# Performance work log

Measured on AMD Instinct MI355X. Metric: run time of the kernel, lower is better.

## Reference

```python
import jax, jax.numpy as jnp
import numpy as np

LOG_EPS = -50.0  # clip_weights lower bound assumption (avoid -inf log-weights)

B, T, P, D, DOBS = 32, 64, 2048, 32, 16


def setup_inputs() -> dict:
    key = jax.random.key(0)
    k_obs, k_p0, k_A, k_ls, k_C = jax.random.split(key, 5)
    observations = jax.random.normal(k_obs, (B, T, DOBS), dtype=jnp.float32)
    init_particles = jax.random.normal(k_p0, (B, P, D), dtype=jnp.float32)
    # stable-ish linear-Gaussian transition params
    A = 0.9 * jnp.eye(D, dtype=jnp.float32) + 0.02 * jax.random.normal(k_A, (D, D), dtype=jnp.float32)
    b = jnp.zeros((D,), dtype=jnp.float32)
    log_sigma = -1.0 + 0.1 * jax.random.normal(k_ls, (D,), dtype=jnp.float32)
    C = 0.3 * jax.random.normal(k_C, (DOBS, D), dtype=jnp.float32)
    log_r = jnp.zeros((DOBS,), dtype=jnp.float32)
    return {"observations": observations, "init_particles": init_particles,
            "A": A, "b": b, "log_sigma": log_sigma, "C": C, "log_r": log_r}


def _pf_scan(observations, init_particles, A, b, log_sigma, C, log_r):
    Bv, Tv, dim_obs = observations.shape
    Pv = init_particles.shape[1]
    base_key = jax.random.key(42)
    # initial weights: ones/P, as in get_initial_state (normalized to log-uniform in step)
    w0 = jnp.full((Bv, Pv, 1), 1.0 / Pv, dtype=init_particles.dtype)
    obs_t = jnp.swapaxes(observations, 0, 1)  # [T,B,obs]
    log2pi = jnp.log(2.0 * jnp.pi).astype(init_particles.dtype)

    def step(carry, xs):
        particles, weights = carry
        t, y = xs
        k = jax.random.fold_in(base_key, t)
        k_res, k_noise = jax.random.split(k)
        # _normalize: log-space normalize + clip
        w = weights - jax.scipy.special.logsumexp(weights, axis=1, keepdims=True)
        w = jnp.maximum(w, LOG_EPS)
        # _resample: categorical over particles, batched gather
        idx = jax.random.categorical(k_res, w[..., 0], shape=(Pv, Bv)).T  # [B,P] int
        particles = jnp.take_along_axis(particles, idx[..., None], axis=1)
        # _forward: linear-Gaussian transition x' = A x + b + sigma*eps
        noise = jax.random.normal(k_noise, particles.shape, dtype=particles.dtype)
        particles = jnp.einsum('bpd,ed->bpe', particles, A) + b + noise * jnp.exp(log_sigma)
        # _measurement: log N(y; C x, diag(exp(log_r)^2))  -> [B,P,1]
        mean = jnp.einsum('bpd,od->bpo', particles, C)
        resid = (y[:, None, :] - mean) * jnp.exp(-log_r)
        logw = (-0.5 * jnp.sum(resid * resid, axis=-1)
                - jnp.sum(log_r) - 0.5 * dim_obs * log2pi)
        weights = logw[..., None]
        return (particles, weights), (particles, weights)

    (_, _), (pseq, wseq) = jax.lax.scan(step, (init_particles, w0),
                                        (jnp.arange(Tv), obs_t))
    # [T,B,...] -> [B,T,...]
    return jnp.swapaxes(pseq, 0, 1), jnp.swapaxes(wseq, 0, 1)


def reference(observations, init_particles, A, b, log_sigma, C, log_r):
    return _pf_scan(observations, init_particles, A, b, log_sigma, C, log_r)
```

## Files before the change

kernel.cpp:

```cpp
#include <hip/hip_runtime.h>
#include <math.h>

#define Bb 32
#define Tt 64
#define Pp 2048
#define Dd 32
#define NOBS 16

__device__ __forceinline__ unsigned rotl32(unsigned v, int r) {
  return (v << r) | (v >> (32 - r));
}

__device__ __forceinline__ void tf2x32(unsigned k0, unsigned k1,
                                       unsigned c0, unsigned c1,
                                       unsigned& r0, unsigned& r1) {
  unsigned k2 = k0 ^ k1 ^ 0x1BD11BDAu;
  unsigned x0 = c0 + k0;
  unsigned x1 = c1 + k1;
#define TF_ROUND(R) { x0 += x1; x1 = rotl32(x1, (R)); x1 ^= x0; }
  TF_ROUND(13) TF_ROUND(15) TF_ROUND(26) TF_ROUND(6)
  x0 += k1; x1 += k2 + 1u;
  TF_ROUND(17) TF_ROUND(29) TF_ROUND(16) TF_ROUND(24)
  x0 += k2; x1 += k0 + 2u;
  TF_ROUND(13) TF_ROUND(15) TF_ROUND(26) TF_ROUND(6)
  x0 += k0; x1 += k1 + 3u;
  TF_ROUND(17) TF_ROUND(29) TF_ROUND(16) TF_ROUND(24)
  x0 += k1; x1 += k2 + 4u;
  TF_ROUND(13) TF_ROUND(15) TF_ROUND(26) TF_ROUND(6)
  x0 += k2; x1 += k0 + 5u;
#undef TF_ROUND
  r0 = x0; r1 = x1;
}

__device__ __forceinline__ float logf_cr(float x) { return (float)log((double)x); }
__device__ __forceinline__ float expf_cr(float x) { return (float)exp((double)x); }

__device__ __forceinline__ float gumbel_exact(unsigned bits) {
  float fl = __uint_as_float(0x3f800000u | (bits >> 9)) - 1.0f;
  float u  = __fadd_rn(fl, 1.17549435e-38f);
  float il = logf_cr(u);
  return -logf_cr(-il);
}

__device__ __forceinline__ float gumbel_fast(unsigned bits) {
  float fl = __uint_as_float(0x3f800000u | (bits >> 9)) - 1.0f;
  if (fl > 0.999877929f) return gumbel_exact(bits);
  float u  = fl + 1.17549435e-38f;
  float t  = -__log2f(u);
  return fmaf(-0.69314718056f, __log2f(t), 0.3665129205816643f);
}

__device__ __forceinline__ float erfinv_xla(float x) {
  float nxx = __fmul_rn(-x, x);
  float l1p;
  if (fabsf(nxx) < 1e-4f) {
    l1p = __fmul_rn(__fadd_rn(__fmul_rn(-0.5f, nxx), 1.0f), nxx);
  } else {
    l1p = logf_cr(__fadd_rn(1.0f, nxx));
  }
  float w = -l1p;
  float p;
  if (w < 5.0f) {
    float ww = __fsub_rn(w, 2.5f);
    p = 2.81022636e-08f;
    p = __fadd_rn(3.43273939e-07f,  __fmul_rn(p, ww));
    p = __fadd_rn(-3.5233877e-06f,  __fmul_rn(p, ww));
    p = __fadd_rn(-4.39150654e-06f, __fmul_rn(p, ww));
    p = __fadd_rn(0.00021858087f,   __fmul_rn(p, ww));
    p = __fadd_rn(-0.00125372503f,  __fmul_rn(p, ww));
    p = __fadd_rn(-0.00417768164f,  __fmul_rn(p, ww));
    p = __fadd_rn(0.246640727f,     __fmul_rn(p, ww));
    p = __fadd_rn(1.50140941f,      __fmul_rn(p, ww));
  } else {
    float ww = __fsub_rn(sqrtf(w), 3.0f);
    p = -0.000200214257f;
    p = __fadd_rn(0.000100950558f,  __fmul_rn(p, ww));
    p = __fadd_rn(0.00134934322f,   __fmul_rn(p, ww));
    p = __fadd_rn(-0.00367342844f,  __fmul_rn(p, ww));
    p = __fadd_rn(0.00573950773f,   __fmul_rn(p, ww));
    p = __fadd_rn(-0.0076224613f,   __fmul_rn(p, ww));
    p = __fadd_rn(0.00943887047f,   __fmul_rn(p, ww));
    p = __fadd_rn(1.00167406f,      __fmul_rn(p, ww));
    p = __fadd_rn(2.83297682f,      __fmul_rn(p, ww));
  }
  return __fmul_rn(p, x);
}

__global__ __launch_bounds__(256) void norm_kernel(float* __restrict__ wseq,
                                                   int t) {
  __shared__ float lw[Pp];
  __shared__ float red[256];
  __shared__ float rr[128];
  __shared__ float sh_mx, sh_lse;
  int b = blockIdx.x;
  int tid = threadIdx.x;
  const float* src = wseq + ((size_t)b * Tt + (t - 1)) * Pp;
  float loc[8];
  for (int k = 0; k < 8; ++k) {
    int j = tid + k * 256;
    float v = (t == 0) ? 0.00048828125f : src[j];
    lw[j] = v; loc[k] = v;
  }
  float m = loc[0];
  for (int k = 1; k < 8; ++k) m = fmaxf(m, loc[k]);
  red[tid] = m;
  __syncthreads();
  if (tid == 0) {
    float mm = red[0];
    for (int k = 1; k < 256; ++k) mm = fmaxf(mm, red[k]);
    sh_mx = mm;
  }
  __syncthreads();
  float mx = sh_mx;
  if (tid < 128) {
    int base = (tid >> 3) * 128 + (tid & 7);
    float r = expf_cr(__fsub_rn(lw[base], mx));
    for (int i = 1; i < 16; ++i)
      r = __fadd_rn(r, expf_cr(__fsub_rn(lw[base + 8 * i], mx)));
    rr[tid] = r;
  }
  __syncthreads();
  if (tid < 64) {
    float s = __fadd_rn(rr[2 * tid], rr[2 * tid + 1]);
    for (int off = 1; off <= 32; off <<= 1)
      s = __fadd_rn(s, __shfl_xor(s, off));
    if (tid == 0) sh_lse = __fadd_rn(logf_cr(s), mx);
  }
  __syncthreads();
  float lse = sh_lse;
  float* dst = wseq + ((size_t)b * Tt + t) * Pp;
  for (int k = 0; k < 8; ++k) {
    int j = tid + k * 256;
    dst[j] = fmaxf(__fsub_rn(lw[j], lse), -50.0f);
  }
}

__global__ __launch_bounds__(256) void cat_kernel(const float* __restrict__ wseq,
                                                  float* __restrict__ pseq,
                                                  int t) {
  __shared__ float wlds[Pp];
  int b = blockIdx.y;
  int tid = threadIdx.x;
  const float* wn = wseq + ((size_t)b * Tt + t) * Pp;
  for (int k = 0; k < Pp / 256; ++k)
    wlds[tid + k * 256] = wn[tid + k * 256];
  __syncthreads();

  unsigned kt0, kt1, kr0, kr1;
  tf2x32(0u, 42u, 0u, (unsigned)t, kt0, kt1);
  tf2x32(kt0, kt1, 0u, 0u, kr0, kr1);

  int wave = tid >> 6, lane = tid & 63;
  int i = blockIdx.x * 4 + wave;
  unsigned base_m = ((unsigned)i * Bb + (unsigned)b) * (unsigned)Pp;

  float vf[32];
  float best = -INFINITY;
#pragma unroll
  for (int jj = 0; jj < 32; ++jj) {
    unsigned b0, b1;
    tf2x32(kr0, kr1, 0u, base_m + (unsigned)(jj * 64 + lane), b0, b1);
    float v = __fadd_rn(gumbel_fast(b0 ^ b1), wlds[jj * 64 + lane]);
    vf[jj] = v;
    best = fmaxf(best, v);
  }
  for (int off = 1; off <= 32; off <<= 1)
    best = fmaxf(best, __shfl_xor(best, off));
  float cut = best - 0.125f;

  unsigned mask = 0u;
#pragma unroll
  for (int jj = 0; jj < 32; ++jj)
    mask |= (vf[jj] >= cut) ? (1u << jj) : 0u;

  float bv = -INFINITY;
  int bj = 0x7fffffff;
  while (mask) {
    int jj = __builtin_ctz(mask);
    mask &= mask - 1u;
    int j = jj * 64 + lane;
    unsigned b0, b1;
    tf2x32(kr0, kr1, 0u, base_m + (unsigned)j, b0, b1);
    float v = __fadd_rn(gumbel_exact(b0 ^ b1), wlds[j]);
    if (v > bv) { bv = v; bj = j; }
  }
  for (int off = 1; off <= 32; off <<= 1) {
    float ov = __shfl_xor(bv, off);
    int   oj = __shfl_xor(bj, off);
    if (ov > bv || (ov == bv && oj < bj)) { bv = ov; bj = oj; }
  }
  if (lane == 0)
    ((int*)pseq)[(((size_t)b * Tt + t) * Pp + i) * Dd] = bj;
}

__global__ __launch_bounds__(256) void fwd_kernel(
    const float* __restrict__ prev,
    float* __restrict__ pseq,
    float* __restrict__ wseq,
    const float* __restrict__ obs,
    const float* __restrict__ Amat,
    const float* __restrict__ bvec,
    const float* __restrict__ log_sigma,
    const float* __restrict__ Cmat,
    const float* __restrict__ log_r,
    int t) {
  int gid = blockIdx.x * 256 + threadIdx.x;
  int b = gid >> 11;
  int p = gid & (Pp - 1);

  unsigned kt0, kt1, kn0, kn1;
  tf2x32(0u, 42u, 0u, (unsigned)t, kt0, kt1);
  tf2x32(kt0, kt1, 0u, 1u, kn0, kn1);

  size_t slot = (((size_t)b * Tt + t) * Pp + p) * Dd;
  int src_p = ((const int*)pseq)[slot];
  const float* xsrc = (t == 0)
      ? (prev + ((size_t)b * Pp + src_p) * Dd)
      : (prev + (((size_t)b * Tt + (t - 1)) * Pp + src_p) * Dd);
  float x[Dd];
  for (int d = 0; d < Dd; ++d) x[d] = xsrc[d];

  float xn[Dd];
  unsigned base_m = ((unsigned)b * Pp + (unsigned)p) * (unsigned)Dd;
  for (int e = 0; e < Dd; ++e) {
    float acc = 0.f;
    for (int d = 0; d < Dd; ++d) acc = fmaf(x[d], Amat[e * Dd + d], acc);
    unsigned b0, b1;
    tf2x32(kn0, kn1, 0u, base_m + (unsigned)e, b0, b1);
    unsigned bits = b0 ^ b1;
    float fl = __uint_as_float(0x3f800000u | (bits >> 9)) - 1.0f;
    float u  = __fadd_rn(__fmul_rn(fl, 2.0f), -0x1.fffffep-1f);
    float n  = __fmul_rn(1.41421356f, erfinv_xla(u));
    xn[e] = __fadd_rn(__fadd_rn(acc, bvec[e]),
                      __fmul_rn(n, expf_cr(log_sigma[e])));
  }

  float* pdst = pseq + slot;
  for (int e = 0; e < Dd; ++e) pdst[e] = xn[e];

  const float* y = obs + ((size_t)b * Tt + t) * NOBS;
  float aa[NOBS];
  for (int o = 0; o < NOBS; ++o) {
    float macc = 0.f;
    for (int d = 0; d < Dd; ++d) macc = fmaf(xn[d], Cmat[o * Dd + d], macc);
    float r = __fmul_rn(__fsub_rn(y[o], macc), expf_cr(-log_r[o]));
    aa[o] = __fmul_rn(r, r);
  }
  float r8[8], l8[8];
  for (int o = 0; o < 8; ++o) {
    r8[o] = __fadd_rn(aa[o], aa[o + 8]);
    l8[o] = __fadd_rn(log_r[o], log_r[o + 8]);
  }
  float S = __fadd_rn(
      __fadd_rn(__fadd_rn(r8[0], r8[1]), __fadd_rn(r8[2], r8[3])),
      __fadd_rn(__fadd_rn(r8[4], r8[5]), __fadd_rn(r8[6], r8[7])));
  float slr = __fadd_rn(
      __fadd_rn(__fadd_rn(l8[0], l8[1]), __fadd_rn(l8[2], l8[3])),
      __fadd_rn(__fadd_rn(l8[4], l8[5]), __fadd_rn(l8[6], l8[7])));
  const float c_term = 8.0f * (float)1.8378770664093453;
  float logw = __fsub_rn(__fsub_rn(__fmul_rn(-0.5f, S), slr), c_term);
  wseq[((size_t)b * Tt + t) * Pp + p] = logw;
}

extern "C" void kernel_launch(void* const* d_in, const int* in_sizes, int n_in,
                              void* d_out, int out_size, void* d_ws, size_t ws_size,
                              hipStream_t stream) {
  (void)in_sizes; (void)n_in; (void)out_size; (void)d_ws; (void)ws_size;
  const float* obs       = (const float*)d_in[0];
  const float* init_p    = (const float*)d_in[1];
  const float* Amat      = (const float*)d_in[2];
  const float* bvec      = (const float*)d_in[3];
  const float* log_sigma = (const float*)d_in[4];
  const float* Cmat      = (const float*)d_in[5];
  const float* log_r     = (const float*)d_in[6];

  float* pseq = (float*)d_out;
  float* wseq = pseq + (size_t)Bb * Tt * Pp * Dd;

  for (int t = 0; t < Tt; ++t) {
    norm_kernel<<<Bb, 256, 0, stream>>>(wseq, t);
    cat_kernel<<<dim3(Pp / 4, Bb), 256, 0, stream>>>(wseq, pseq, t);
    fwd_kernel<<<(Bb * Pp) / 256, 256, 0, stream>>>(
        t == 0 ? init_p : pseq, pseq, wseq,
        obs, Amat, bvec, log_sigma, Cmat, log_r, t);
  }
}
```

Before: 23.28 ms.

## Prune resampling candidates whose log-weight cannot win the Gumbel-max draw

The normalization kernel now keeps only particles whose normalized log-weight is within a fixed margin (20.45) of the maximum. It compacts them with a shared-memory atomic counter into a (weight, index) workspace list, along with a per-batch count. The categorical kernel loads only those active entries and runs the Threefry and Gumbel evaluations over whole 64-wide chunks of them, padding the tail with -inf. The aim is to skip most of the per-candidate RNG and Gumbel cost when the weights are peaked. Results stay exact only if the margin exceeds the spread of Gumbel noise that float uniforms can produce; atomic ordering is nondeterministic, so ties are broken explicitly by index.

Result: no change. 23.62 ms (+1.4%).

```diff
diff --git a/kernel.cpp b/kernel.cpp
--- a/kernel.cpp
+++ b/kernel.cpp
@@ -86,12 +86,15 @@
   return __fmul_rn(p, x);
 }
 
-__global__ __launch_bounds__(256) void norm_kernel(float* __restrict__ wseq,
+__global__ __launch_bounds__(256) void norm_kernel(const float* __restrict__ wseq,
+                                                   float2* __restrict__ act,
+                                                   int* __restrict__ counts,
                                                    int t) {
   __shared__ float lw[Pp];
   __shared__ float red[256];
   __shared__ float rr[128];
   __shared__ float sh_mx, sh_lse;
+  __shared__ int s_cnt;
   int b = blockIdx.x;
   int tid = threadIdx.x;
   const float* src = wseq + ((size_t)b * Tt + (t - 1)) * Pp;
@@ -126,24 +129,37 @@
       s = __fadd_rn(s, __shfl_xor(s, off));
     if (tid == 0) sh_lse = __fadd_rn(logf_cr(s), mx);
   }
+  if (tid == 0) s_cnt = 0;
   __syncthreads();
   float lse = sh_lse;
-  float* dst = wseq + ((size_t)b * Tt + t) * Pp;
+  float thr = __fsub_rn(__fsub_rn(mx, lse), 20.45f);
+  float2* abase = act + (size_t)b * Pp;
   for (int k = 0; k < 8; ++k) {
     int j = tid + k * 256;
-    dst[j] = fmaxf(__fsub_rn(lw[j], lse), -50.0f);
-  }
-}
-
-__global__ __launch_bounds__(256) void cat_kernel(const float* __restrict__ wseq,
+    float wn = fmaxf(__fsub_rn(lw[j], lse), -50.0f);
+    if (wn >= thr) {
+      int pos = atomicAdd(&s_cnt, 1);
+      abase[pos] = make_float2(wn, __int_as_float(j));
+    }
+  }
+  __syncthreads();
+  if (tid == 0) counts[b] = s_cnt;
+}
+
+__global__ __launch_bounds__(256) void cat_kernel(const float2* __restrict__ act,
+                                                  const int* __restrict__ counts,
                                                   float* __restrict__ pseq,
                                                   int t) {
-  __shared__ float wlds[Pp];
+  __shared__ float2 alds[Pp];
   int b = blockIdx.y;
   int tid = threadIdx.x;
-  const float* wn = wseq + ((size_t)b * Tt + t) * Pp;
-  for (int k = 0; k < Pp / 256; ++k)
-    wlds[tid + k * 256] = wn[tid + k * 256];
+  int n_act = counts[b];
+  int nchunk = (n_act + 63) >> 6;
+  int tot = nchunk << 6;
+  const float2* abase = act + (size_t)b * Pp;
+  for (int k = tid; k < tot; k += 256)
+    alds[k] = (k < n_act) ? abase[k]
+                          : make_float2(-INFINITY, __int_as_float(0x7fffffff));
   __syncthreads();
 
   unsigned kt0, kt1, kr0, kr1;
@@ -157,12 +173,17 @@
   float vf[32];
   float best = -INFINITY;
 #pragma unroll
-  for (int jj = 0; jj < 32; ++jj) {
-    unsigned b0, b1;
-    tf2x32(kr0, kr1, 0u, base_m + (unsigned)(jj * 64 + lane), b0, b1);
-    float v = __fadd_rn(gumbel_fast(b0 ^ b1), wlds[jj * 64 + lane]);
-    vf[jj] = v;
-    best = fmaxf(best, v);
+  for (int c = 0; c < 32; ++c) {
+    if (c < nchunk) {
+      float2 aw = alds[c * 64 + lane];
+      unsigned b0, b1;
+      tf2x32(kr0, kr1, 0u, base_m + (unsigned)__float_as_int(aw.y), b0, b1);
+      float v = __fadd_rn(gumbel_fast(b0 ^ b1), aw.x);
+      vf[c] = v;
+      best = fmaxf(best, v);
+    } else {
+      vf[c] = -INFINITY;
+    }
   }
   for (int off = 1; off <= 32; off <<= 1)
     best = fmaxf(best, __shfl_xor(best, off));
@@ -170,19 +191,20 @@
 
   unsigned mask = 0u;
 #pragma unroll
-  for (int jj = 0; jj < 32; ++jj)
-    mask |= (vf[jj] >= cut) ? (1u << jj) : 0u;
+  for (int c = 0; c < 32; ++c)
+    mask |= (vf[c] >= cut) ? (1u << c) : 0u;
 
   float bv = -INFINITY;
   int bj = 0x7fffffff;
   while (mask) {
-    int jj = __builtin_ctz(mask);
+    int c = __builtin_ctz(mask);
     mask &= mask - 1u;
-    int j = jj * 64 + lane;
+    float2 aw = alds[c * 64 + lane];
+    int j = __float_as_int(aw.y);
     unsigned b0, b1;
     tf2x32(kr0, kr1, 0u, base_m + (unsigned)j, b0, b1);
-    float v = __fadd_rn(gumbel_exact(b0 ^ b1), wlds[j]);
-    if (v > bv) { bv = v; bj = j; }
+    float v = __fadd_rn(gumbel_exact(b0 ^ b1), aw.x);
+    if (v > bv || (v == bv && j < bj)) { bv = v; bj = j; }
   }
   for (int off = 1; off <= 32; off <<= 1) {
     float ov = __shfl_xor(bv, off);
@@ -265,7 +287,7 @@
 extern "C" void kernel_launch(void* const* d_in, const int* in_sizes, int n_in,
                               void* d_out, int out_size, void* d_ws, size_t ws_size,
                               hipStream_t stream) {
-  (void)in_sizes; (void)n_in; (void)out_size; (void)d_ws; (void)ws_size;
+  (void)in_sizes; (void)n_in; (void)out_size; (void)ws_size;
   const float* obs       = (const float*)d_in[0];
   const float* init_p    = (const float*)d_in[1];
   const float* Amat      = (const float*)d_in[2];
@@ -277,9 +299,12 @@
   float* pseq = (float*)d_out;
   float* wseq = pseq + (size_t)Bb * Tt * Pp * Dd;
 
+  int*    counts = (int*)d_ws;
+  float2* act    = (float2*)((char*)d_ws + 256);
+
   for (int t = 0; t < Tt; ++t) {
-    norm_kernel<<<Bb, 256, 0, stream>>>(wseq, t);
-    cat_kernel<<<dim3(Pp / 4, Bb), 256, 0, stream>>>(wseq, pseq, t);
+    norm_kernel<<<Bb, 256, 0, stream>>>(wseq, act, counts, t);
+    cat_kernel<<<dim3(Pp / 4, Bb), 256, 0, stream>>>(act, counts, pseq, t);
     fwd_kernel<<<(Bb * Pp) / 256, 256, 0, stream>>>(
         t == 0 ? init_p : pseq, pseq, wseq,
         obs, Amat, bvec, log_sigma, Cmat, log_r, t);
```

## Prefilter Gumbel-max candidates via precomputed integer thresholds on random bits

Applied to the files above, without the earlier changes.

The normalize kernel now writes the normalized log-weights plus, for each particle, the smallest raw random-bit value whose Gumbel sample would push weight+Gumbel above a fixed cutoff. The categorical kernel then only generates Threefry bits and does an integer compare per candidate, computing exact Gumbel logs only for the few that pass, instead of a fast Gumbel for every candidate. If no candidate reaches the cutoff, a full exact rescan runs as a fallback, so results stay exact. PRNG key derivation per timestep also moves to the host and is passed as kernel arguments, at the cost of an extra workspace array and more double-precision math in the normalize kernel.

New measurement: 23.23 ms. Within noise of the previous version (-0.2%).

```diff
diff --git a/kernel.cpp b/kernel.cpp
--- a/kernel.cpp
+++ b/kernel.cpp
@@ -6,6 +6,8 @@
 #define Pp 2048
 #define Dd 32
 #define NOBS 16
+
+#define CUTF (-2.3f)
 
 __device__ __forceinline__ unsigned rotl32(unsigned v, int r) {
   return (v << r) | (v >> (32 - r));
@@ -32,6 +34,27 @@
   r0 = x0; r1 = x1;
 }
 
+static inline void tf2x32_host(unsigned k0, unsigned k1,
+                               unsigned c0, unsigned c1,
+                               unsigned& r0, unsigned& r1) {
+  unsigned k2 = k0 ^ k1 ^ 0x1BD11BDAu;
+  unsigned x0 = c0 + k0;
+  unsigned x1 = c1 + k1;
+#define TF_ROUND(R) { x0 += x1; x1 = (x1 << (R)) | (x1 >> (32 - (R))); x1 ^= x0; }
+  TF_ROUND(13) TF_ROUND(15) TF_ROUND(26) TF_ROUND(6)
+  x0 += k1; x1 += k2 + 1u;
+  TF_ROUND(17) TF_ROUND(29) TF_ROUND(16) TF_ROUND(24)
+  x0 += k2; x1 += k0 + 2u;
+  TF_ROUND(13) TF_ROUND(15) TF_ROUND(26) TF_ROUND(6)
+  x0 += k0; x1 += k1 + 3u;
+  TF_ROUND(17) TF_ROUND(29) TF_ROUND(16) TF_ROUND(24)
+  x0 += k1; x1 += k2 + 4u;
+  TF_ROUND(13) TF_ROUND(15) TF_ROUND(26) TF_ROUND(6)
+  x0 += k2; x1 += k0 + 5u;
+#undef TF_ROUND
+  r0 = x0; r1 = x1;
+}
+
 __device__ __forceinline__ float logf_cr(float x) { return (float)log((double)x); }
 __device__ __forceinline__ float expf_cr(float x) { return (float)exp((double)x); }
 
@@ -40,14 +63,6 @@
   float u  = __fadd_rn(fl, 1.17549435e-38f);
   float il = logf_cr(u);
   return -logf_cr(-il);
-}
-
-__device__ __forceinline__ float gumbel_fast(unsigned bits) {
-  float fl = __uint_as_float(0x3f800000u | (bits >> 9)) - 1.0f;
-  if (fl > 0.999877929f) return gumbel_exact(bits);
-  float u  = fl + 1.17549435e-38f;
-  float t  = -__log2f(u);
-  return fmaf(-0.69314718056f, __log2f(t), 0.3665129205816643f);
 }
 
 __device__ __forceinline__ float erfinv_xla(float x) {
@@ -86,7 +101,9 @@
   return __fmul_rn(p, x);
 }
 
-__global__ __launch_bounds__(256) void norm_kernel(float* __restrict__ wseq,
+__global__ __launch_bounds__(256) void norm_kernel(const float* __restrict__ wseq,
+                                                   float* __restrict__ wn_out,
+                                                   unsigned* __restrict__ vs_out,
                                                    int t) {
   __shared__ float lw[Pp];
   __shared__ float red[256];
@@ -128,67 +145,88 @@
   }
   __syncthreads();
   float lse = sh_lse;
-  float* dst = wseq + ((size_t)b * Tt + t) * Pp;
+  float* wdst = wn_out + (size_t)b * Pp;
+  unsigned* vdst = vs_out + (size_t)b * Pp;
   for (int k = 0; k < 8; ++k) {
     int j = tid + k * 256;
-    dst[j] = fmaxf(__fsub_rn(lw[j], lse), -50.0f);
-  }
-}
-
-__global__ __launch_bounds__(256) void cat_kernel(const float* __restrict__ wseq,
+    float wn = fmaxf(__fsub_rn(lw[j], lse), -50.0f);
+    wdst[j] = wn;
+    double g_req = (double)CUTF - (double)wn;
+    double U  = exp(-exp(-g_req));
+    double Um = U - 1e-4;
+    unsigned V;
+    if (!(Um > 0.0)) {
+      V = 0u;
+    } else {
+      double mth = ceil(Um * 8388608.0);
+      V = (mth >= 8388608.0) ? 0xFFFFFFFFu : (((unsigned)mth) << 9);
+    }
+    vdst[j] = V;
+  }
+}
+
+__global__ __launch_bounds__(256) void cat_kernel(const float* __restrict__ wn_ws,
+                                                  const unsigned* __restrict__ vs_ws,
                                                   float* __restrict__ pseq,
-                                                  int t) {
+                                                  int t, unsigned kr0, unsigned kr1) {
   __shared__ float wlds[Pp];
+  __shared__ unsigned vlds[Pp];
   int b = blockIdx.y;
   int tid = threadIdx.x;
-  const float* wn = wseq + ((size_t)b * Tt + t) * Pp;
-  for (int k = 0; k < Pp / 256; ++k)
-    wlds[tid + k * 256] = wn[tid + k * 256];
-  __syncthreads();
-
-  unsigned kt0, kt1, kr0, kr1;
-  tf2x32(0u, 42u, 0u, (unsigned)t, kt0, kt1);
-  tf2x32(kt0, kt1, 0u, 0u, kr0, kr1);
+  const float*    wsrc = wn_ws + (size_t)b * Pp;
+  const unsigned* vsrc = vs_ws + (size_t)b * Pp;
+  for (int k = 0; k < Pp / 256; ++k) {
+    wlds[tid + k * 256] = wsrc[tid + k * 256];
+    vlds[tid + k * 256] = vsrc[tid + k * 256];
+  }
+  __syncthreads();
 
   int wave = tid >> 6, lane = tid & 63;
   int i = blockIdx.x * 4 + wave;
   unsigned base_m = ((unsigned)i * Bb + (unsigned)b) * (unsigned)Pp;
 
-  float vf[32];
-  float best = -INFINITY;
-#pragma unroll
-  for (int jj = 0; jj < 32; ++jj) {
+  unsigned mask = 0u;
+#pragma unroll 4
+  for (int c = 0; c < 32; ++c) {
     unsigned b0, b1;
-    tf2x32(kr0, kr1, 0u, base_m + (unsigned)(jj * 64 + lane), b0, b1);
-    float v = __fadd_rn(gumbel_fast(b0 ^ b1), wlds[jj * 64 + lane]);
-    vf[jj] = v;
-    best = fmaxf(best, v);
-  }
-  for (int off = 1; off <= 32; off <<= 1)
-    best = fmaxf(best, __shfl_xor(best, off));
-  float cut = best - 0.125f;
-
-  unsigned mask = 0u;
-#pragma unroll
-  for (int jj = 0; jj < 32; ++jj)
-    mask |= (vf[jj] >= cut) ? (1u << jj) : 0u;
+    tf2x32(kr0, kr1, 0u, base_m + (unsigned)(c * 64 + lane), b0, b1);
+    unsigned bits = b0 ^ b1;
+    if (bits >= vlds[c * 64 + lane]) mask |= (1u << c);
+  }
 
   float bv = -INFINITY;
   int bj = 0x7fffffff;
   while (mask) {
-    int jj = __builtin_ctz(mask);
+    int c = __builtin_ctz(mask);
     mask &= mask - 1u;
-    int j = jj * 64 + lane;
+    int j = c * 64 + lane;
     unsigned b0, b1;
     tf2x32(kr0, kr1, 0u, base_m + (unsigned)j, b0, b1);
     float v = __fadd_rn(gumbel_exact(b0 ^ b1), wlds[j]);
-    if (v > bv) { bv = v; bj = j; }
+    if (v > bv || (v == bv && j < bj)) { bv = v; bj = j; }
   }
   for (int off = 1; off <= 32; off <<= 1) {
     float ov = __shfl_xor(bv, off);
     int   oj = __shfl_xor(bj, off);
     if (ov > bv || (ov == bv && oj < bj)) { bv = ov; bj = oj; }
   }
+
+  if (!(bv >= CUTF)) {
+    bv = -INFINITY; bj = 0x7fffffff;
+    for (int c = 0; c < 32; ++c) {
+      int j = c * 64 + lane;
+      unsigned b0, b1;
+      tf2x32(kr0, kr1, 0u, base_m + (unsigned)j, b0, b1);
+      float v = __fadd_rn(gumbel_exact(b0 ^ b1), wlds[j]);
+      if (v > bv || (v == bv && j < bj)) { bv = v; bj = j; }
+    }
+    for (int off = 1; off <= 32; off <<= 1) {
+      float ov = __shfl_xor(bv, off);
+      int   oj = __shfl_xor(bj, off);
+      if (ov > bv || (ov == bv && oj < bj)) { bv = ov; bj = oj; }
+    }
+  }
+
   if (lane == 0)
     ((int*)pseq)[(((size_t)b * Tt + t) * Pp + i) * Dd] = bj;
 }
@@ -203,14 +241,10 @@
     const float* __restrict__ log_sigma,
     const float* __restrict__ Cmat,
     const float* __restrict__ log_r,
-    int t) {
+    int t, unsigned kn0, unsigned kn1) {
   int gid = blockIdx.x * 256 + threadIdx.x;
   int b = gid >> 11;
   int p = gid & (Pp - 1);
-
-  unsigned kt0, kt1, kn0, kn1;
-  tf2x32(0u, 42u, 0u, (unsigned)t, kt0, kt1);
-  tf2x32(kt0, kt1, 0u, 1u, kn0, kn1);
 
   size_t slot = (((size_t)b * Tt + t) * Pp + p) * Dd;
   int src_p = ((const int*)pseq)[slot];
@@ -265,7 +299,7 @@
 extern "C" void kernel_launch(void* const* d_in, const int* in_sizes, int n_in,
                               void* d_out, int out_size, void* d_ws, size_t ws_size,
                               hipStream_t stream) {
-  (void)in_sizes; (void)n_in; (void)out_size; (void)d_ws; (void)ws_size;
+  (void)in_sizes; (void)n_in; (void)out_size; (void)ws_size;
   const float* obs       = (const float*)d_in[0];
   const float* init_p    = (const float*)d_in[1];
   const float* Amat      = (const float*)d_in[2];
@@ -277,11 +311,19 @@
   float* pseq = (float*)d_out;
   float* wseq = pseq + (size_t)Bb * Tt * Pp * Dd;
 
+  float*    wn = (float*)d_ws;
+  unsigned* vs = (unsigned*)((char*)d_ws + (size_t)Bb * Pp * 4);
+
   for (int t = 0; t < Tt; ++t) {
-    norm_kernel<<<Bb, 256, 0, stream>>>(wseq, t);
-    cat_kernel<<<dim3(Pp / 4, Bb), 256, 0, stream>>>(wseq, pseq, t);
+    unsigned kt0, kt1, kr0, kr1, kn0, kn1;
+    tf2x32_host(0u, 42u, 0u, (unsigned)t, kt0, kt1);
+    tf2x32_host(kt0, kt1, 0u, 0u, kr0, kr1);
+    tf2x32_host(kt0, kt1, 0u, 1u, kn0, kn1);
+
+    norm_kernel<<<Bb, 256, 0, stream>>>(wseq, wn, vs, t);
+    cat_kernel<<<dim3(Pp / 4, Bb), 256, 0, stream>>>(wn, vs, pseq, t, kr0, kr1);
     fwd_kernel<<<(Bb * Pp) / 256, 256, 0, stream>>>(
         t == 0 ? init_p : pseq, pseq, wseq,
-        obs, Amat, bvec, log_sigma, Cmat, log_r, t);
-  }
-}
+        obs, Amat, bvec, log_sigma, Cmat, log_r, t, kn0, kn1);
+  }
+}
```
